# Optimization experiments

Measured on AMD Instinct MI355X. Metric: run time of the kernel, lower is better.

Reference implementation:

```python
import jax, jax.numpy as jnp
import numpy as np

QA = 4  # quaternion dimension (qa in the torch code)


def _bingham_sample(lam, key):
    """ACG rejection sampler for Bingham(lam), lam > 0, shape [N, 4].
    Faithful to bingham_rj: resample rejected rows until all accepted.
    Implemented with a fixed-shape lax.while_loop (resample everything,
    keep accepted rows via where) so it is jit-compatible."""
    sigacginv = 1.0 + 2.0 * lam            # [N,4]
    sig = jnp.sqrt(1.0 / sigacginv)        # SigACG, per-component std
    N = lam.shape[0]
    X0 = jnp.zeros((N, QA), lam.dtype)
    acc0 = jnp.zeros((N,), dtype=bool)

    half_qa = QA / 2.0
    log_qa = jnp.log(jnp.asarray(QA, lam.dtype))

    def cond(state):
        _, acc, _ = state
        return ~jnp.all(acc)

    def body(state):
        X, acc, key = state
        key, k1, k2 = jax.random.split(key, 3)
        yp = jax.random.normal(k1, (N, QA), lam.dtype) * sig
        y = yp / jnp.linalg.norm(yp, axis=1, keepdims=True)
        y2 = y * y
        lratio = (-jnp.sum(y2 * lam, axis=1)
                  - half_qa * log_qa
                  + 0.5 * (QA - 1)
                  + half_qa * jnp.log(jnp.sum(y2 * sigacginv, axis=1)))
        u = jax.random.uniform(k2, (N,), lam.dtype)
        # torch code: X[indx] = y (overwrite not-yet-accepted), then decide accept
        X = jnp.where(acc[:, None], X, y)
        acc = acc | (jnp.log(u) < lratio)
        return X, acc, key

    X, _, _ = jax.lax.while_loop(cond, body, (X0, acc0, key))
    return X


def _make_E(qn):
    """Build z_Q [N,4,4] from unit quaternions, exactly as reparameterize_rj."""
    q0, q1, q2, q3 = qn[:, 0], qn[:, 1], qn[:, 2], qn[:, 3]
    r1 = jnp.stack([q0, -q1, -q2, q3], axis=-1)
    r2 = jnp.stack([q1, q0, q3, q2], axis=-1)
    r3 = jnp.stack([q2, -q3, q0, -q1], axis=-1)
    r4 = jnp.stack([q3, q2, -q1, -q0], axis=-1)
    return jnp.stack([r1, r2, r3, r4], axis=1)  # rows stacked along dim 1


def setup_inputs() -> dict:
    key = jax.random.key(0)
    kq, kz = jax.random.split(key)
    N = 1048576
    q = jax.random.normal(kq, (N, 4), jnp.float32)
    # strictly negative, monotonically decreasing concentrations (Z0<Z1<Z2 in |.|)
    dZ = jax.random.uniform(kz, (N, 3), jnp.float32, minval=1e-3, maxval=100.0)
    Zbatch = -jnp.cumsum(dZ, axis=1)  # [N,3], all < 0
    return {"q": q, "Zbatch": Zbatch, "seed": 42}


def reference(q, Zbatch, seed):
    # F.normalize on the quaternion output (done in forward before reparameterize_rj)
    qn = q / jnp.linalg.norm(q, axis=1, keepdims=True)
    E = _make_E(qn)                                              # [N,4,4]
    N = q.shape[0]
    Zexp = jnp.concatenate(
        [jnp.full((N, 1), -1e-6, Zbatch.dtype), Zbatch], axis=1)  # [N,4], all < 0
    lam = -Zexp                                                   # lam > 0
    X = _bingham_sample(lam, jax.random.key(seed))                # [N,4]
    # torch.bmm(E.transpose(1,2), X.unsqueeze(2)).squeeze() == E^T @ x per row
    return jnp.einsum('nij,ni->nj', E, X)
```

## Files before the change

kernel.cpp:

```cpp
#include <hip/hip_runtime.h>
#include <cstdint>


#define DEVI __device__ __forceinline__
#define MAXT 96
#define GRID 512
#define NT 256
#define CMAX 2048

DEVI uint32_t rotl32(uint32_t v, int s) { return (v << s) | (v >> (32 - s)); }

DEVI void tf2x32(uint32_t k0, uint32_t k1, uint32_t x0, uint32_t x1,
                 uint32_t& o0, uint32_t& o1) {
  const uint32_t kx = k0 ^ k1 ^ 0x1BD11BDAu;
  x0 += k0; x1 += k1;
#define TFR(r) x0 += x1; x1 = rotl32(x1, (r)); x1 ^= x0;
  TFR(13) TFR(15) TFR(26) TFR(6)
  x0 += k1; x1 += kx + 1u;
  TFR(17) TFR(29) TFR(16) TFR(24)
  x0 += kx; x1 += k0 + 2u;
  TFR(13) TFR(15) TFR(26) TFR(6)
  x0 += k0; x1 += k1 + 3u;
  TFR(17) TFR(29) TFR(16) TFR(24)
  x0 += k1; x1 += kx + 4u;
  TFR(13) TFR(15) TFR(26) TFR(6)
  x0 += kx; x1 += k0 + 5u;
#undef TFR
  o0 = x0; o1 = x1;
}

DEVI void tf_round5(uint32_t x0[5], uint32_t x1[5], int rr) {
#pragma unroll
  for (int j = 0; j < 5; ++j) {
    x0[j] += x1[j];
    x1[j] = rotl32(x1[j], rr);
    x1[j] ^= x0[j];
  }
}
DEVI void tf_inj5(uint32_t x0[5], uint32_t x1[5],
                  const uint32_t* sa, const uint32_t* sb, uint32_t add) {
#pragma unroll
  for (int j = 0; j < 5; ++j) { x0[j] += sa[j]; x1[j] += sb[j] + add; }
}

DEVI float u01_from_bits(uint32_t bits) {
  return __fsub_rn(__uint_as_float(0x3f800000u | (bits >> 9)), 1.0f);
}

DEVI void trial5(uint4 ck, uint32_t base, uint32_t ctr, float u[5]) {
  uint32_t s0[5], s1[5], s2k[5], x0[5], x1[5];
#pragma unroll
  for (int j = 0; j < 5; ++j) {
    uint32_t k0 = (j < 4) ? ck.x : ck.z;
    uint32_t k1 = (j < 4) ? ck.y : ck.w;
    s0[j] = k0; s1[j] = k1; s2k[j] = k0 ^ k1 ^ 0x1BD11BDAu;
    uint32_t c = (j < 4) ? (base + (uint32_t)j) : ctr;
    x0[j] = k0;
    x1[j] = c + k1;
  }
  tf_round5(x0, x1, 13); tf_round5(x0, x1, 15);
  tf_round5(x0, x1, 26); tf_round5(x0, x1, 6);
  tf_inj5(x0, x1, s1, s2k, 1u);
  tf_round5(x0, x1, 17); tf_round5(x0, x1, 29);
  tf_round5(x0, x1, 16); tf_round5(x0, x1, 24);
  tf_inj5(x0, x1, s2k, s0, 2u);
  tf_round5(x0, x1, 13); tf_round5(x0, x1, 15);
  tf_round5(x0, x1, 26); tf_round5(x0, x1, 6);
  tf_inj5(x0, x1, s0, s1, 3u);
  tf_round5(x0, x1, 17); tf_round5(x0, x1, 29);
  tf_round5(x0, x1, 16); tf_round5(x0, x1, 24);
  tf_inj5(x0, x1, s1, s2k, 4u);
  tf_round5(x0, x1, 13); tf_round5(x0, x1, 15);
  tf_round5(x0, x1, 26); tf_round5(x0, x1, 6);
  tf_inj5(x0, x1, s2k, s0, 5u);
#pragma unroll
  for (int j = 0; j < 5; ++j) u[j] = u01_from_bits(x0[j] ^ x1[j]);
}

template <int K>
DEVI void xla_logf_pos_k(const float* xf, float* out) {
  float e[K], m[K], z[K], y[K];
#pragma unroll
  for (int j = 0; j < K; ++j) {
    uint32_t bits = __float_as_uint(xf[j]);
    e[j] = (float)((int)(bits >> 23) - 126);
    m[j] = __uint_as_float((bits & 0x007fffffu) | 0x3f000000u);
    bool mc = m[j] < 0.70710678118654752440f;
    float e_lo = __fsub_rn(e[j], 1.0f);
    float m_lo = __fadd_rn(__fsub_rn(m[j], 1.0f), m[j]);
    float m_hi = __fsub_rn(m[j], 1.0f);
    e[j] = mc ? e_lo : e[j];
    m[j] = mc ? m_lo : m_hi;
    z[j] = __fmul_rn(m[j], m[j]);
    y[j] = 7.0376836292e-2f;
  }
  const float LC[8] = {-1.1514610310e-1f,  1.1676998740e-1f,
                       -1.2420140846e-1f,  1.4249322787e-1f,
                       -1.6668057665e-1f,  2.0000714765e-1f,
                       -2.4999993993e-1f,  3.3333331174e-1f};
#pragma unroll
  for (int s = 0; s < 8; ++s)
#pragma unroll
    for (int j = 0; j < K; ++j)
      y[j] = __fadd_rn(__fmul_rn(y[j], m[j]), LC[s]);
#pragma unroll
  for (int j = 0; j < K; ++j) {
    float t = __fmul_rn(__fmul_rn(y[j], m[j]), z[j]);
    t = __fadd_rn(t, __fmul_rn(e[j], -2.12194440e-4f));
    t = __fsub_rn(t, __fmul_rn(z[j], 0.5f));
    float r = __fadd_rn(m[j], t);
    out[j] = __fadd_rn(r, __fmul_rn(e[j], 0.693359375f));
  }
}

DEVI void xla_erfinv4_logu(const float* xin, float uu, float* res,
                           float& lg_uu) {
  float v[4], vp1[5], big[5], w[4], q[4], p[4];
  bool c[4];
#pragma unroll
  for (int j = 0; j < 4; ++j) {
    v[j] = -__fmul_rn(xin[j], xin[j]);
    vp1[j] = __fadd_rn(v[j], 1.0f);
  }
  vp1[4] = uu;
  xla_logf_pos_k<5>(vp1, big);
  lg_uu = big[4];
#pragma unroll
  for (int j = 0; j < 4; ++j) {
    float small = __fmul_rn(__fadd_rn(__fmul_rn(-0.5f, v[j]), 1.0f), v[j]);
    float l1p = (fabsf(v[j]) < 1e-4f) ? small : big[j];
    w[j] = -l1p;
    c[j] = (w[j] < 5.0f);
    float qc = __fsub_rn(w[j], 2.5f);
    float qr = __fsub_rn(sqrtf(w[j]), 3.0f);
    q[j] = c[j] ? qc : qr;
    p[j] = c[j] ? 2.81022636e-08f : -0.000200214257f;
  }
  const float CF[8] = { 3.43273939e-07f, -3.5233877e-06f, -4.39150654e-06f,
                        0.00021858087f,  -0.00125372503f, -0.00417768164f,
                        0.246640727f,     1.50140941f};
  const float CR[8] = { 0.000100950558f,  0.00134934322f, -0.00367342844f,
                        0.00573950773f,  -0.0076224613f,   0.00943887047f,
                        1.00167406f,      2.83297682f};
#pragma unroll
  for (int s = 0; s < 8; ++s)
#pragma unroll
    for (int j = 0; j < 4; ++j)
      p[j] = __fadd_rn(__fmul_rn(p[j], q[j]), c[j] ? CF[s] : CR[s]);
#pragma unroll
  for (int j = 0; j < 4; ++j) res[j] = __fmul_rn(p[j], xin[j]);
}

__global__ __launch_bounds__(256, 2) void campose_kernel(
    const float* __restrict__ q, const float* __restrict__ Z,
    float* __restrict__ out, const int* __restrict__ seedp, int N, int C) {
  __shared__ uint4 chain[MAXT + 1];
  __shared__ float rowc[CMAX * 6];
  __shared__ uint32_t next_row;
  __shared__ uint32_t wm;

  const int tid = threadIdx.x;
  const int rbeg = blockIdx.x * C;
  const int rend = min(N, rbeg + C);
  const int crows = rend - rbeg;
  if (tid == 0) { next_row = (uint32_t)(rbeg + 192); wm = 0u; }

  for (int i = tid; i < crows; i += NT) {
    float z0 = Z[(size_t)(rbeg + i) * 3 + 0];
    float z1 = Z[(size_t)(rbeg + i) * 3 + 1];
    float z2 = Z[(size_t)(rbeg + i) * 3 + 2];
    float l1 = -z0, l2 = -z1, l3 = -z2;
    float g1 = __fadd_rn(1.0f, __fmul_rn(2.0f, l1));
    float g2 = __fadd_rn(1.0f, __fmul_rn(2.0f, l2));
    float g3 = __fadd_rn(1.0f, __fmul_rn(2.0f, l3));
    float s1_ = sqrtf(__fdiv_rn(1.0f, g1));
    float s2_ = sqrtf(__fdiv_rn(1.0f, g2));
    float s3_ = sqrtf(__fdiv_rn(1.0f, g3));
    rowc[i * 6 + 0] = g1; rowc[i * 6 + 1] = g2; rowc[i * 6 + 2] = g3;
    rowc[i * 6 + 3] = s1_; rowc[i * 6 + 4] = s2_; rowc[i * 6 + 5] = s3_;
  }
  __syncthreads();

  const int wave = tid >> 6;
  if (wave == 0) {
    int lane = tid & 63;
    uint32_t ka = 0u, kb = (uint32_t)seedp[0];
    uint32_t x1i = (lane == 2) ? 0u : (uint32_t)(lane + 1);
    for (int t = 0; t < MAXT; ++t) {
      uint32_t o0 = 0u, o1 = 0u;
      if (lane < 3) tf2x32(ka, kb, 0u, x1i, o0, o1);
      uint32_t s1a = __shfl(o0, 0, 64), s1b = __shfl(o1, 0, 64);
      uint32_t s2a = __shfl(o0, 1, 64), s2b = __shfl(o1, 1, 64);
      if (lane == 0) chain[t] = make_uint4(s1a, s1b, s2a, s2b);
      ka = __shfl(o0, 2, 64); kb = __shfl(o1, 2, 64);
      __threadfence_block();
      if (lane == 0) *(volatile uint32_t*)&wm = (uint32_t)(t + 1);
    }
    if (lane == 0) chain[MAXT] = make_uint4(0u, 0u, 0u, 0u);
    __threadfence_block();
    if (lane == 0) *(volatile uint32_t*)&wm = (uint32_t)(MAXT + 1);
  }

  const float sgi0 = __fadd_rn(1.0f, __fmul_rn(2.0f, 1e-6f));
  const float sig0 = sqrtf(__fdiv_rn(1.0f, sgi0));

  int r, rn;
  if (wave == 0) {
    r  = (int)atomicAdd(&next_row, 1u);
    rn = (int)atomicAdd(&next_row, 1u);
  } else {
    r  = rbeg + (tid - 64);
    rn = (int)atomicAdd(&next_row, 1u);
  }
  bool have = (r < rend);
  float Zn0 = 0, Zn1 = 0, Zn2 = 0;
  float lam1 = 0, lam2 = 0, lam3 = 0;
  float sgi1 = 1, sgi2 = 1, sgi3 = 1;
  float sig1 = 1, sig2 = 1, sig3 = 1;
  if (have) {
    lam1 = -Z[r * 3 + 0]; lam2 = -Z[r * 3 + 1]; lam3 = -Z[r * 3 + 2];
    int li = r - rbeg;
    sgi1 = rowc[li * 6 + 0]; sgi2 = rowc[li * 6 + 1]; sgi3 = rowc[li * 6 + 2];
    sig1 = rowc[li * 6 + 3]; sig2 = rowc[li * 6 + 4]; sig3 = rowc[li * 6 + 5];
  }
  if (rn < rend) { Zn0 = Z[rn * 3 + 0]; Zn1 = Z[rn * 3 + 1]; Zn2 = Z[rn * 3 + 2]; }

  uint32_t wml = *(volatile uint32_t*)&wm;
  while (wml < 1u) wml = *(volatile uint32_t*)&wm;
  __threadfence_block();
  const uint4 ck0 = chain[0];
  uint4 ck = ck0;
  bool chain_all = (wml >= (uint32_t)(MAXT + 1));
  int t = 0;

  while (__ballot(have)) {
    if (have) {
      if (!chain_all) {
        uint32_t need = (uint32_t)(t + 2);
        uint32_t w_ = *(volatile uint32_t*)&wm;
        while (w_ < need) w_ = *(volatile uint32_t*)&wm;
        __threadfence_block();
        chain_all = (w_ >= (uint32_t)(MAXT + 1));
      }
      uint4 ckn = chain[t + 1];

      const uint32_t base = ((uint32_t)r) * 4u;

      float u5[5];
      trial5(ck, base, (uint32_t)r, u5);
      float uu = u5[4];

      float xin[4];
#pragma unroll
      for (int j = 0; j < 4; ++j) {
        float x = __fadd_rn(__fmul_rn(u5[j], 2.0f), -0.99999994f);
        xin[j] = fmaxf(-0.99999994f, x);
      }
      float er[4], lg_uu;
      xla_erfinv4_logu(xin, uu, er, lg_uu);

      float y0 = __fmul_rn(__fmul_rn(1.41421356237309504880f, er[0]), sig0);
      float y1 = __fmul_rn(__fmul_rn(1.41421356237309504880f, er[1]), sig1);
      float y2v = __fmul_rn(__fmul_rn(1.41421356237309504880f, er[2]), sig2);
      float y3 = __fmul_rn(__fmul_rn(1.41421356237309504880f, er[3]), sig3);

      float n2 = __fmul_rn(y0, y0);
      n2 = __fadd_rn(n2, __fmul_rn(y1, y1));
      n2 = __fadd_rn(n2, __fmul_rn(y2v, y2v));
      n2 = __fadd_rn(n2, __fmul_rn(y3, y3));
      float nr = sqrtf(n2);
      y0 = __fdiv_rn(y0, nr); y1 = __fdiv_rn(y1, nr);
      y2v = __fdiv_rn(y2v, nr); y3 = __fdiv_rn(y3, nr);

      float s0q = __fmul_rn(y0, y0), s1q = __fmul_rn(y1, y1);
      float s2q = __fmul_rn(y2v, y2v), s3q = __fmul_rn(y3, y3);

      float s1v = __fmul_rn(s0q, 1e-6f);
      s1v = __fadd_rn(s1v, __fmul_rn(s1q, lam1));
      s1v = __fadd_rn(s1v, __fmul_rn(s2q, lam2));
      s1v = __fadd_rn(s1v, __fmul_rn(s3q, lam3));

      float s2v = __fmul_rn(s0q, sgi0);
      s2v = __fadd_rn(s2v, __fmul_rn(s1q, sgi1));
      s2v = __fadd_rn(s2v, __fmul_rn(s2q, sgi2));
      s2v = __fadd_rn(s2v, __fmul_rn(s3q, sgi3));

      float lg_s2[1];
      xla_logf_pos_k<1>(&s2v, lg_s2);

      float lr = __fsub_rn(-s1v, 2.7725887298583984f);
      lr = __fadd_rn(lr, 1.5f);
      lr = __fadd_rn(lr, __fmul_rn(2.0f, lg_s2[0]));

      float lu = (uu > 0.0f) ? lg_uu : -__builtin_inff();

      ++t;
      if ((lu < lr) || (t >= MAXT)) {
        *reinterpret_cast<float4*>(out + (size_t)r * 4) =
            make_float4(y0, y1, y2v, y3);
        r = rn;
        lam1 = -Zn0; lam2 = -Zn1; lam3 = -Zn2;
        int li = (r < rend ? r : rend - 1) - rbeg;
        sgi1 = rowc[li * 6 + 0]; sgi2 = rowc[li * 6 + 1];
        sgi3 = rowc[li * 6 + 2];
        sig1 = rowc[li * 6 + 3]; sig2 = rowc[li * 6 + 4];
        sig3 = rowc[li * 6 + 5];
        t = 0;
        ck = ck0;
        have = (r < rend);
        rn = (int)atomicAdd(&next_row, 1u);
        if (rn < rend) {
          Zn0 = Z[rn * 3 + 0]; Zn1 = Z[rn * 3 + 1]; Zn2 = Z[rn * 3 + 2];
        }
      } else {
        ck = ckn;
      }
    }
  }

  __syncthreads();
  for (int i = rbeg + tid; i < rend; i += NT) {
    float4 yv = *reinterpret_cast<const float4*>(out + (size_t)i * 4);
    float4 qv = *reinterpret_cast<const float4*>(q + (size_t)i * 4);
    float a = qv.x, b = qv.y, c = qv.z, d = qv.w;
    float qn2 = __fmul_rn(a, a);
    qn2 = __fadd_rn(qn2, __fmul_rn(b, b));
    qn2 = __fadd_rn(qn2, __fmul_rn(c, c));
    qn2 = __fadd_rn(qn2, __fmul_rn(d, d));
    float qnr = sqrtf(qn2);
    a = __fdiv_rn(a, qnr); b = __fdiv_rn(b, qnr);
    c = __fdiv_rn(c, qnr); d = __fdiv_rn(d, qnr);
    float y0 = yv.x, y1 = yv.y, y2v = yv.z, y3 = yv.w;
    float o0v = __fadd_rn(__fadd_rn(__fadd_rn(__fmul_rn(a, y0), __fmul_rn(b, y1)),
                                    __fmul_rn(c, y2v)), __fmul_rn(d, y3));
    float o1v = __fadd_rn(__fadd_rn(__fadd_rn(__fmul_rn(-b, y0), __fmul_rn(a, y1)),
                                    __fmul_rn(-d, y2v)), __fmul_rn(c, y3));
    float o2v = __fadd_rn(__fadd_rn(__fadd_rn(__fmul_rn(-c, y0), __fmul_rn(d, y1)),
                                    __fmul_rn(a, y2v)), __fmul_rn(-b, y3));
    float o3v = __fadd_rn(__fadd_rn(__fadd_rn(__fmul_rn(d, y0), __fmul_rn(c, y1)),
                                    __fmul_rn(-b, y2v)), __fmul_rn(-a, y3));
    *reinterpret_cast<float4*>(out + (size_t)i * 4) =
        make_float4(o0v, o1v, o2v, o3v);
  }
}

extern "C" void kernel_launch(void* const* d_in, const int* in_sizes, int n_in,
                              void* d_out, int out_size, void* d_ws, size_t ws_size,
                              hipStream_t stream) {
  const float* q = (const float*)d_in[0];
  const float* Z = (const float*)d_in[1];
  const int* seed = (const int*)d_in[2];
  float* out = (float*)d_out;
  int N = in_sizes[0] / 4;

  int nb = GRID;
  int C = (N + nb - 1) / nb;
  if (C > CMAX) {
    nb = (N + CMAX - 1) / CMAX;
    C = (N + nb - 1) / nb;
  }
  campose_kernel<<<nb, NT, 0, stream>>>(q, Z, out, seed, N, C);
}
```

Before: 187.7 us.

## Switch to gang-parallel trial evaluation when few lanes remain active in rejection loop

When a wavefront's active row count drops to GANGA or below, the kernel leaves the per-lane rejection loop. It then evaluates up to four consecutive trials of one row across a gang of four lanes, with up to 16 rows per wave in parallel, and picks the first accepted trial by ballot. The aim is to cut the long tail where only a few lanes keep iterating while the rest of the wave idles. Per-row lambda values now sit in a structure-of-arrays shared buffer instead of being reloaded from global memory, which removes the prefetch of Z for the next row. In exchange there is extra speculative work in the tail and more complex lane bookkeeping that must preserve the exact trial order.

```diff
diff --git a/kernel.cpp b/kernel.cpp
--- a/kernel.cpp
+++ b/kernel.cpp
@@ -7,6 +7,9 @@
 #define GRID 512
 #define NT 256
 #define CMAX 2048
+#define GANGA 56
+#define NG 16
+#define GW 4
 
 DEVI uint32_t rotl32(uint32_t v, int s) { return (v << s) | (v >> (32 - s)); }
 
@@ -151,15 +154,76 @@
   for (int j = 0; j < 4; ++j) res[j] = __fmul_rn(p[j], xin[j]);
 }
 
+DEVI bool trial_eval(uint4 ck, int r,
+                     float lam1, float lam2, float lam3,
+                     float sgi1, float sgi2, float sgi3,
+                     float sig1, float sig2, float sig3,
+                     float sgi0, float sig0,
+                     float& ry0, float& ry1, float& ry2, float& ry3) {
+  const uint32_t base = ((uint32_t)r) * 4u;
+
+  float u5[5];
+  trial5(ck, base, (uint32_t)r, u5);
+  float uu = u5[4];
+
+  float xin[4];
+#pragma unroll
+  for (int j = 0; j < 4; ++j) {
+    float x = __fadd_rn(__fmul_rn(u5[j], 2.0f), -0.99999994f);
+    xin[j] = fmaxf(-0.99999994f, x);
+  }
+  float er[4], lg_uu;
+  xla_erfinv4_logu(xin, uu, er, lg_uu);
+
+  float y0 = __fmul_rn(__fmul_rn(1.41421356237309504880f, er[0]), sig0);
+  float y1 = __fmul_rn(__fmul_rn(1.41421356237309504880f, er[1]), sig1);
+  float y2v = __fmul_rn(__fmul_rn(1.41421356237309504880f, er[2]), sig2);
+  float y3 = __fmul_rn(__fmul_rn(1.41421356237309504880f, er[3]), sig3);
+
+  float n2 = __fmul_rn(y0, y0);
+  n2 = __fadd_rn(n2, __fmul_rn(y1, y1));
+  n2 = __fadd_rn(n2, __fmul_rn(y2v, y2v));
+  n2 = __fadd_rn(n2, __fmul_rn(y3, y3));
+  float nr = sqrtf(n2);
+  y0 = __fdiv_rn(y0, nr); y1 = __fdiv_rn(y1, nr);
+  y2v = __fdiv_rn(y2v, nr); y3 = __fdiv_rn(y3, nr);
+
+  float s0q = __fmul_rn(y0, y0), s1q = __fmul_rn(y1, y1);
+  float s2q = __fmul_rn(y2v, y2v), s3q = __fmul_rn(y3, y3);
+
+  float s1v = __fmul_rn(s0q, 1e-6f);
+  s1v = __fadd_rn(s1v, __fmul_rn(s1q, lam1));
+  s1v = __fadd_rn(s1v, __fmul_rn(s2q, lam2));
+  s1v = __fadd_rn(s1v, __fmul_rn(s3q, lam3));
+
+  float s2v = __fmul_rn(s0q, sgi0);
+  s2v = __fadd_rn(s2v, __fmul_rn(s1q, sgi1));
+  s2v = __fadd_rn(s2v, __fmul_rn(s2q, sgi2));
+  s2v = __fadd_rn(s2v, __fmul_rn(s3q, sgi3));
+
+  float lg_s2[1];
+  xla_logf_pos_k<1>(&s2v, lg_s2);
+
+  float lr = __fsub_rn(-s1v, 2.7725887298583984f);
+  lr = __fadd_rn(lr, 1.5f);
+  lr = __fadd_rn(lr, __fmul_rn(2.0f, lg_s2[0]));
+
+  float lu = (uu > 0.0f) ? lg_uu : -__builtin_inff();
+
+  ry0 = y0; ry1 = y1; ry2 = y2v; ry3 = y3;
+  return (lu < lr);
+}
+
 __global__ __launch_bounds__(256, 2) void campose_kernel(
     const float* __restrict__ q, const float* __restrict__ Z,
     float* __restrict__ out, const int* __restrict__ seedp, int N, int C) {
   __shared__ uint4 chain[MAXT + 1];
-  __shared__ float rowc[CMAX * 6];
+  __shared__ float rc[9][CMAX];
   __shared__ uint32_t next_row;
   __shared__ uint32_t wm;
 
   const int tid = threadIdx.x;
+  const int lane = tid & 63;
   const int rbeg = blockIdx.x * C;
   const int rend = min(N, rbeg + C);
   const int crows = rend - rbeg;
@@ -176,14 +240,14 @@
     float s1_ = sqrtf(__fdiv_rn(1.0f, g1));
     float s2_ = sqrtf(__fdiv_rn(1.0f, g2));
     float s3_ = sqrtf(__fdiv_rn(1.0f, g3));
-    rowc[i * 6 + 0] = g1; rowc[i * 6 + 1] = g2; rowc[i * 6 + 2] = g3;
-    rowc[i * 6 + 3] = s1_; rowc[i * 6 + 4] = s2_; rowc[i * 6 + 5] = s3_;
+    rc[0][i] = g1; rc[1][i] = g2; rc[2][i] = g3;
+    rc[3][i] = s1_; rc[4][i] = s2_; rc[5][i] = s3_;
+    rc[6][i] = l1; rc[7][i] = l2; rc[8][i] = l3;
   }
   __syncthreads();
 
   const int wave = tid >> 6;
   if (wave == 0) {
-    int lane = tid & 63;
     uint32_t ka = 0u, kb = (uint32_t)seedp[0];
     uint32_t x1i = (lane == 2) ? 0u : (uint32_t)(lane + 1);
     for (int t = 0; t < MAXT; ++t) {
@@ -213,108 +277,112 @@
     rn = (int)atomicAdd(&next_row, 1u);
   }
   bool have = (r < rend);
-  float Zn0 = 0, Zn1 = 0, Zn2 = 0;
   float lam1 = 0, lam2 = 0, lam3 = 0;
   float sgi1 = 1, sgi2 = 1, sgi3 = 1;
   float sig1 = 1, sig2 = 1, sig3 = 1;
   if (have) {
-    lam1 = -Z[r * 3 + 0]; lam2 = -Z[r * 3 + 1]; lam3 = -Z[r * 3 + 2];
     int li = r - rbeg;
-    sgi1 = rowc[li * 6 + 0]; sgi2 = rowc[li * 6 + 1]; sgi3 = rowc[li * 6 + 2];
-    sig1 = rowc[li * 6 + 3]; sig2 = rowc[li * 6 + 4]; sig3 = rowc[li * 6 + 5];
-  }
-  if (rn < rend) { Zn0 = Z[rn * 3 + 0]; Zn1 = Z[rn * 3 + 1]; Zn2 = Z[rn * 3 + 2]; }
+    sgi1 = rc[0][li]; sgi2 = rc[1][li]; sgi3 = rc[2][li];
+    sig1 = rc[3][li]; sig2 = rc[4][li]; sig3 = rc[5][li];
+    lam1 = rc[6][li]; lam2 = rc[7][li]; lam3 = rc[8][li];
+  }
 
   uint32_t wml = *(volatile uint32_t*)&wm;
   while (wml < 1u) wml = *(volatile uint32_t*)&wm;
   __threadfence_block();
   const uint4 ck0 = chain[0];
   uint4 ck = ck0;
-  bool chain_all = (wml >= (uint32_t)(MAXT + 1));
   int t = 0;
 
-  while (__ballot(have)) {
+  while (true) {
+    uint64_t msk = __ballot(have);
+    if (__popcll(msk) <= GANGA) break;
     if (have) {
-      if (!chain_all) {
-        uint32_t need = (uint32_t)(t + 2);
+      if (wml < (uint32_t)(t + 2)) {
         uint32_t w_ = *(volatile uint32_t*)&wm;
-        while (w_ < need) w_ = *(volatile uint32_t*)&wm;
+        while (w_ < (uint32_t)(t + 2)) w_ = *(volatile uint32_t*)&wm;
         __threadfence_block();
-        chain_all = (w_ >= (uint32_t)(MAXT + 1));
+        wml = w_;
       }
       uint4 ckn = chain[t + 1];
 
-      const uint32_t base = ((uint32_t)r) * 4u;
-
-      float u5[5];
-      trial5(ck, base, (uint32_t)r, u5);
-      float uu = u5[4];
-
-      float xin[4];
-#pragma unroll
-      for (int j = 0; j < 4; ++j) {
-        float x = __fadd_rn(__fmul_rn(u5[j], 2.0f), -0.99999994f);
-        xin[j] = fmaxf(-0.99999994f, x);
-      }
-      float er[4], lg_uu;
-      xla_erfinv4_logu(xin, uu, er, lg_uu);
-
-      float y0 = __fmul_rn(__fmul_rn(1.41421356237309504880f, er[0]), sig0);
-      float y1 = __fmul_rn(__fmul_rn(1.41421356237309504880f, er[1]), sig1);
-      float y2v = __fmul_rn(__fmul_rn(1.41421356237309504880f, er[2]), sig2);
-      float y3 = __fmul_rn(__fmul_rn(1.41421356237309504880f, er[3]), sig3);
-
-      float n2 = __fmul_rn(y0, y0);
-      n2 = __fadd_rn(n2, __fmul_rn(y1, y1));
-      n2 = __fadd_rn(n2, __fmul_rn(y2v, y2v));
-      n2 = __fadd_rn(n2, __fmul_rn(y3, y3));
-      float nr = sqrtf(n2);
-      y0 = __fdiv_rn(y0, nr); y1 = __fdiv_rn(y1, nr);
-      y2v = __fdiv_rn(y2v, nr); y3 = __fdiv_rn(y3, nr);
-
-      float s0q = __fmul_rn(y0, y0), s1q = __fmul_rn(y1, y1);
-      float s2q = __fmul_rn(y2v, y2v), s3q = __fmul_rn(y3, y3);
-
-      float s1v = __fmul_rn(s0q, 1e-6f);
-      s1v = __fadd_rn(s1v, __fmul_rn(s1q, lam1));
-      s1v = __fadd_rn(s1v, __fmul_rn(s2q, lam2));
-      s1v = __fadd_rn(s1v, __fmul_rn(s3q, lam3));
-
-      float s2v = __fmul_rn(s0q, sgi0);
-      s2v = __fadd_rn(s2v, __fmul_rn(s1q, sgi1));
-      s2v = __fadd_rn(s2v, __fmul_rn(s2q, sgi2));
-      s2v = __fadd_rn(s2v, __fmul_rn(s3q, sgi3));
-
-      float lg_s2[1];
-      xla_logf_pos_k<1>(&s2v, lg_s2);
-
-      float lr = __fsub_rn(-s1v, 2.7725887298583984f);
-      lr = __fadd_rn(lr, 1.5f);
-      lr = __fadd_rn(lr, __fmul_rn(2.0f, lg_s2[0]));
-
-      float lu = (uu > 0.0f) ? lg_uu : -__builtin_inff();
+      float y0, y1, y2v, y3;
+      bool alr = trial_eval(ck, r, lam1, lam2, lam3, sgi1, sgi2, sgi3,
+                            sig1, sig2, sig3, sgi0, sig0, y0, y1, y2v, y3);
 
       ++t;
-      if ((lu < lr) || (t >= MAXT)) {
+      if (alr || (t >= MAXT)) {
         *reinterpret_cast<float4*>(out + (size_t)r * 4) =
             make_float4(y0, y1, y2v, y3);
         r = rn;
-        lam1 = -Zn0; lam2 = -Zn1; lam3 = -Zn2;
         int li = (r < rend ? r : rend - 1) - rbeg;
-        sgi1 = rowc[li * 6 + 0]; sgi2 = rowc[li * 6 + 1];
-        sgi3 = rowc[li * 6 + 2];
-        sig1 = rowc[li * 6 + 3]; sig2 = rowc[li * 6 + 4];
-        sig3 = rowc[li * 6 + 5];
+        sgi1 = rc[0][li]; sgi2 = rc[1][li]; sgi3 = rc[2][li];
+        sig1 = rc[3][li]; sig2 = rc[4][li]; sig3 = rc[5][li];
+        lam1 = rc[6][li]; lam2 = rc[7][li]; lam3 = rc[8][li];
         t = 0;
         ck = ck0;
         have = (r < rend);
         rn = (int)atomicAdd(&next_row, 1u);
-        if (rn < rend) {
-          Zn0 = Z[rn * 3 + 0]; Zn1 = Z[rn * 3 + 1]; Zn2 = Z[rn * 3 + 2];
-        }
       } else {
         ck = ckn;
       }
+    }
+  }
+
+  uint64_t mask = __ballot(have);
+  if (mask) {
+    if (wml < (uint32_t)(MAXT + 1)) {
+      uint32_t w_ = *(volatile uint32_t*)&wm;
+      while (w_ < (uint32_t)(MAXT + 1)) w_ = *(volatile uint32_t*)&wm;
+      __threadfence_block();
+      wml = w_;
+    }
+    while (mask) {
+      int G = __popcll(mask); if (G > NG) G = NG;
+      const int g = lane >> 2, k = lane & 3;
+      const bool gact = (g < G);
+      const int gidx = gact ? g : 0;
+      uint64_t m = mask;
+      int sl = __ffsll((unsigned long long)m) - 1;
+#pragma unroll
+      for (int i = 1; i < NG; ++i) {
+        m &= m - 1;
+        int b = __ffsll((unsigned long long)m) - 1;
+        sl = (i <= gidx && b >= 0) ? b : sl;
+      }
+      int rg = __shfl(r, sl, 64);
+      int tg = __shfl(t, sl, 64);
+      int li = rg - rbeg;
+      float G1 = rc[0][li], G2 = rc[1][li], G3 = rc[2][li];
+      float S1 = rc[3][li], S2 = rc[4][li], S3 = rc[5][li];
+      float L1 = rc[6][li], L2 = rc[7][li], L3 = rc[8][li];
+      int ts = tg + k;
+      int tsc = ts < (MAXT - 1) ? ts : (MAXT - 1);
+      uint4 cks = chain[tsc];
+      float y0, y1, y2v, y3;
+      bool alr = trial_eval(cks, rg, L1, L2, L3, G1, G2, G3,
+                            S1, S2, S3, sgi0, sig0, y0, y1, y2v, y3);
+      bool acc = alr || (ts >= MAXT - 1);
+      uint64_t bal = __ballot(acc && gact);
+      uint64_t gb = (bal >> (g * GW)) & 0xfull;
+      int kwin = gb ? (__ffsll((unsigned long long)gb) - 1) : GW;
+      if (gact && k == kwin) {
+        *reinterpret_cast<float4*>(out + (size_t)rg * 4) =
+            make_float4(y0, y1, y2v, y3);
+      }
+      int myidx = __popcll(mask & ((1ull << lane) - 1ull));
+      if (have && myidx < G) {
+        uint64_t gbb = (bal >> (myidx * GW)) & 0xfull;
+        if (gbb) {
+          r = rn;
+          t = 0;
+          have = (r < rend);
+          rn = (int)atomicAdd(&next_row, 1u);
+        } else {
+          t += GW;
+        }
+      }
+      mask = __ballot(have);
     }
   }
 
```

Result: faster. 155.6 us (-17.1%).
